# Performance work log

Hardware: AMD Instinct MI355X
Metric: run time of the kernel (lower is better)

Reference implementation:

```python
import jax, jax.numpy as jnp
import numpy as np

B, NB, H, C = 32, 1024, 768, 64


def setup_inputs() -> dict:
    key = jax.random.key(0)
    k1, k2, k3, k4, k5, k6 = jax.random.split(key, 6)
    block_tokens = jax.random.normal(k1, (B, NB, H), dtype=jnp.float32)
    block_active = jax.random.randint(k2, (B, NB), 0, 2) == 1
    block_to_channel_map = jax.random.randint(k3, (NB,), 0, C, dtype=jnp.int64)
    # agg_gate params: Linear(H, H//2) -> Tanh -> Linear(H//2, 1)
    s1 = 1.0 / np.sqrt(H)
    s2 = 1.0 / np.sqrt(H // 2)
    W1 = jax.random.uniform(k4, (H, H // 2), jnp.float32, -s1, s1)
    b1 = jnp.zeros((H // 2,), jnp.float32)
    W2 = jax.random.uniform(k5, (H // 2, 1), jnp.float32, -s2, s2)
    b2 = jnp.zeros((1,), jnp.float32)
    return {"block_tokens": block_tokens, "block_active": block_active,
            "block_to_channel_map": block_to_channel_map,
            "W1": W1, "b1": b1, "W2": W2, "b2": b2}


def reference(block_tokens, block_active, block_to_channel_map, W1, b1, W2, b2):
    # gate MLP: (B, NB)
    h = jnp.tanh(jnp.einsum('bnh,hk->bnk', block_tokens, W1) + b1)
    gate = (jnp.einsum('bnk,ko->bno', h, W2) + b2).squeeze(-1)  # (B, NB)

    # (C, NB) one-hot channel membership; (B, C, NB) active-per-channel mask
    onehot = block_to_channel_map[None, :] == jnp.arange(C)[:, None]
    mask = block_active[:, None, :] & onehot[None, :, :]  # (B, C, NB)

    neg_inf = jnp.float32(-jnp.inf)
    g = jnp.where(mask, gate[:, None, :], neg_inf)  # (B, C, NB)
    m = jnp.max(g, axis=-1, keepdims=True)
    m_safe = jnp.where(jnp.isfinite(m), m, 0.0)  # guard all-masked channels
    e = jnp.where(mask, jnp.exp(g - m_safe), 0.0)
    s = jnp.sum(e, axis=-1, keepdims=True)
    w = jnp.where(s > 0, e / jnp.where(s > 0, s, 1.0), 0.0)  # softmax, nan->0

    channel_tokens = jnp.einsum('bcn,bnh->bch', w, block_tokens)  # (B, C, H)
    channel_active = jnp.any(mask, axis=-1)  # (B, C)
    return channel_tokens, channel_active
```

## Files before the change

### kernel.cpp

```cpp
#include <hip/hip_runtime.h>
#include <math.h>

#define B_    32
#define NB_   1024
#define H_    768
#define K_    384
#define C_    64
#define ROWS_ 32
#define NSTEP_ 24

typedef __attribute__((ext_vector_type(8))) short bf16x8;
typedef __attribute__((ext_vector_type(4))) float f32x4;

__device__ __forceinline__ short f2bf(float f) {
    unsigned u = __float_as_uint(f);
    unsigned r = (u + 0x7fffu + ((u >> 16) & 1u)) >> 16;
    return (short)r;
}
__device__ __forceinline__ float ftanh(float x) {
    float e = __expf(2.f * x);
    return 1.f - 2.f * __builtin_amdgcn_rcpf(e + 1.f);
}

__global__ __launch_bounds__(256) void prep_w1(const float* __restrict__ W1,
                                               short* __restrict__ swz)
{
    int idx = blockIdx.x * 256 + threadIdx.x;
    int k = idx / K_, n = idx % K_;
    float v = W1[idx];
    int s = k >> 5, g = (k >> 3) & 3, i = k & 7;
    int t = n >> 4, nn = n & 15;
    swz[((s * 24 + t) * 512) + (g * 16 + nn) * 8 + i] = f2bf(v);
}

__global__ __launch_bounds__(1024) void compact_kernel(
    const int* __restrict__ active, int* __restrict__ list, int* __restrict__ cnt)
{
    __shared__ int wsum[16];
    __shared__ int wbase[17];
    const int b = blockIdx.x, tid = threadIdx.x, lane = tid & 63, wid = tid >> 6;
    const int flag = active[b * NB_ + tid] != 0;
    const unsigned long long m = __ballot(flag);
    if (lane == 0) wsum[wid] = __popcll(m);
    __syncthreads();
    if (tid == 0) {
        int r = 0;
        for (int i = 0; i < 16; ++i) { wbase[i] = r; r += wsum[i]; }
        wbase[16] = r;
        cnt[b] = r;
    }
    __syncthreads();
    const int total = wbase[16];
    if (flag) {
        const int pos = wbase[wid] + __popcll(m & ((1ull << lane) - 1ull));
        list[b * NB_ + pos] = tid;
    }
    if (tid >= total) list[b * NB_ + tid] = 0;
}

__global__ __launch_bounds__(256, 3) void gate_kernel(
    const float* __restrict__ tokens, const short* __restrict__ swz,
    const float* __restrict__ b1, const float* __restrict__ W2,
    const float* __restrict__ b2, const int* __restrict__ list,
    const int* __restrict__ cnt, float* __restrict__ gate)
{
    __shared__ __align__(16) short As[NSTEP_ * 1024];
    __shared__ float red[4][32];

    const int b = blockIdx.x >> 5;
    const int chunk = blockIdx.x & 31;
    if (chunk * ROWS_ >= cnt[b]) return;

    const int tid = threadIdx.x;
    const int lane = tid & 63;
    const int w = tid >> 6;

    const int r   = tid >> 3;
    const int c8  = tid & 7;
    const int g2w = c8 >> 1, hw = c8 & 1;
    const int fw  = r >> 4,  roww = r & 15;
    const int woff = ((fw * 4 + g2w) * 16 + (roww ^ (g2w << 1))) * 8 + hw * 4;
    const int nrow = list[b * NB_ + chunk * ROWS_ + r];
    const float* aptr = tokens + ((size_t)b * NB_ + nrow) * H_ + c8 * 4;

    const int g2r  = lane >> 4;
    const int rowr = (lane & 15) ^ (g2r << 1);
    const int roff0 = ((0 + g2r) * 16 + rowr) * 8;
    const int roff1 = ((4 + g2r) * 16 + rowr) * 8;

    const short* bbase = swz + (w * 6) * 512 + lane * 8;

    bf16x8 bs[3][6];
#pragma unroll
    for (int j = 0; j < 6; ++j)
        bs[0][j] = *(const bf16x8*)(bbase + 0 * 12288 + j * 512);
#pragma unroll
    for (int j = 0; j < 6; ++j)
        bs[1][j] = *(const bf16x8*)(bbase + 1 * 12288 + j * 512);

#pragma unroll
    for (int g = 0; g < 4; ++g) {
        float4 pa[6];
#pragma unroll
        for (int q = 0; q < 6; ++q)
            pa[q] = *(const float4*)(aptr + (g * 6 + q) * 32);
#pragma unroll
        for (int q = 0; q < 6; ++q) {
            short4 av = {f2bf(pa[q].x), f2bf(pa[q].y), f2bf(pa[q].z), f2bf(pa[q].w)};
            *(short4*)&As[(g * 6 + q) * 1024 + woff] = av;
        }
    }

    f32x4 acc[6][2];
#pragma unroll
    for (int j = 0; j < 6; ++j)
#pragma unroll
        for (int f = 0; f < 2; ++f) acc[j][f] = (f32x4){0.f, 0.f, 0.f, 0.f};

    __syncthreads();

#pragma unroll
    for (int s = 0; s < NSTEP_; ++s) {
        if (s + 2 < NSTEP_) {
            const short* bp = bbase + (size_t)(s + 2) * 12288;
#pragma unroll
            for (int j = 0; j < 6; ++j)
                bs[(s + 2) % 3][j] = *(const bf16x8*)(bp + j * 512);
        }
        bf16x8 a0 = *(const bf16x8*)&As[s * 1024 + roff0];
        bf16x8 a1 = *(const bf16x8*)&As[s * 1024 + roff1];
#pragma unroll
        for (int j = 0; j < 6; ++j) {
            acc[j][0] = __builtin_amdgcn_mfma_f32_16x16x32_bf16(
                            a0, bs[s % 3][j], acc[j][0], 0, 0, 0);
            acc[j][1] = __builtin_amdgcn_mfma_f32_16x16x32_bf16(
                            a1, bs[s % 3][j], acc[j][1], 0, 0, 0);
        }
    }

    float ps[2][4];
#pragma unroll
    for (int f = 0; f < 2; ++f)
#pragma unroll
        for (int rr = 0; rr < 4; ++rr) ps[f][rr] = 0.f;

#pragma unroll
    for (int j = 0; j < 6; ++j) {
        const int n = (w * 6 + j) * 16 + (lane & 15);
        const float bb = b1[n];
        const float ww = W2[n];
#pragma unroll
        for (int f = 0; f < 2; ++f)
#pragma unroll
            for (int rr = 0; rr < 4; ++rr)
                ps[f][rr] += ftanh(acc[j][f][rr] + bb) * ww;
    }
#pragma unroll
    for (int m = 1; m < 16; m <<= 1)
#pragma unroll
        for (int f = 0; f < 2; ++f)
#pragma unroll
            for (int rr = 0; rr < 4; ++rr)
                ps[f][rr] += __shfl_xor(ps[f][rr], m, 64);

    if ((lane & 15) == 0) {
        const int rbase = (lane >> 4) * 4;
#pragma unroll
        for (int f = 0; f < 2; ++f)
#pragma unroll
            for (int rr = 0; rr < 4; ++rr)
                red[w][f * 16 + rbase + rr] = ps[f][rr];
    }
    __syncthreads();
    if (tid < ROWS_) {
        float sg = b2[0];
#pragma unroll
        for (int q = 0; q < 4; ++q) sg += red[q][tid];
        gate[b * NB_ + list[b * NB_ + chunk * ROWS_ + tid]] = sg;
    }
}

__global__ __launch_bounds__(256) void agg_kernel(
    const float* __restrict__ tokens, const int* __restrict__ active,
    const int* __restrict__ cmap, const float* __restrict__ gate,
    float* __restrict__ out_tok, float* __restrict__ out_act)
{
    __shared__ float wls[NB_];
    __shared__ float red[256];
    __shared__ int   idxs[NB_];
    __shared__ float wts[NB_];
    __shared__ int   gbase[17];

    const int b = blockIdx.x >> 6, c = blockIdx.x & 63;
    const int tid = threadIdx.x, lane = tid & 63, wid = tid >> 6;

    float lmax = -INFINITY;
    for (int n = tid; n < NB_; n += 256) {
        const bool msk = (active[b * NB_ + n] != 0) && (cmap[n] == c);
        const float g  = msk ? gate[b * NB_ + n] : -INFINITY;
        wls[n] = g;
        lmax = fmaxf(lmax, g);
    }
    red[tid] = lmax; __syncthreads();
    for (int s = 128; s > 0; s >>= 1) {
        if (tid < s) red[tid] = fmaxf(red[tid], red[tid + s]);
        __syncthreads();
    }
    const float m = red[0]; __syncthreads();
    const float msafe = (m > -INFINITY) ? m : 0.f;

    float lsum = 0.f;
    for (int n = tid; n < NB_; n += 256) {
        const float g = wls[n];
        const float e = (g > -INFINITY) ? __expf(g - msafe) : 0.f;
        wls[n] = e; lsum += e;
    }
    red[tid] = lsum; __syncthreads();
    for (int s = 128; s > 0; s >>= 1) {
        if (tid < s) red[tid] += red[tid + s];
        __syncthreads();
    }
    const float ssum = red[0];
    const float inv  = (ssum > 0.f) ? 1.f / ssum : 0.f;
    __syncthreads();

#pragma unroll
    for (int it = 0; it < 4; ++it) {
        const int n = it * 256 + wid * 64 + lane;
        const unsigned long long mask = __ballot(wls[n] > 0.f);
        if (lane == 0) gbase[1 + it * 4 + wid] = __popcll(mask);
    }
    __syncthreads();
    if (tid == 0) {
        gbase[0] = 0;
        for (int i = 1; i <= 16; ++i) gbase[i] += gbase[i - 1];
    }
    __syncthreads();
#pragma unroll
    for (int it = 0; it < 4; ++it) {
        const int n = it * 256 + wid * 64 + lane;
        const float e = wls[n];
        const unsigned long long mask = __ballot(e > 0.f);
        if (e > 0.f) {
            const int pos = gbase[it * 4 + wid] +
                            __popcll(mask & ((1ull << lane) - 1ull));
            idxs[pos] = n;
            wts[pos]  = e * inv;
        }
    }
    __syncthreads();
    const int cnt = gbase[16];

    if (tid < 192) {
        const int d = tid * 4;
        const float* tb = tokens + (size_t)b * NB_ * H_ + d;
        float4 a = {0.f, 0.f, 0.f, 0.f};
        for (int i = 0; i < cnt; ++i) {
            const float wv = wts[i];
            const float4 v = *(const float4*)(tb + (size_t)idxs[i] * H_);
            a.x += wv * v.x; a.y += wv * v.y;
            a.z += wv * v.z; a.w += wv * v.w;
        }
        *(float4*)(out_tok + ((size_t)(b * C_ + c)) * H_ + d) = a;
    }
    if (tid == 0) out_act[b * C_ + c] = (m > -INFINITY) ? 1.f : 0.f;
}

extern "C" void kernel_launch(void* const* d_in, const int* in_sizes, int n_in,
                              void* d_out, int out_size, void* d_ws, size_t ws_size,
                              hipStream_t stream)
{
    const float* tokens = (const float*)d_in[0];
    const int*   active = (const int*)  d_in[1];
    const int*   cmap   = (const int*)  d_in[2];
    const float* W1     = (const float*)d_in[3];
    const float* b1     = (const float*)d_in[4];
    const float* W2     = (const float*)d_in[5];
    const float* b2     = (const float*)d_in[6];

    float* out      = (float*)d_out;
    float* out_act  = out + (size_t)B_ * C_ * H_;

    short* swz     = (short*)d_ws;
    float* gate_ws = (float*)((char*)d_ws + 589824);
    int*   list    = (int*)  ((char*)d_ws + 720896);
    int*   cntb    = (int*)  ((char*)d_ws + 851968);

    compact_kernel<<<B_, 1024, 0, stream>>>(active, list, cntb);
    prep_w1<<<(H_ * K_) / 256, 256, 0, stream>>>(W1, swz);
    gate_kernel<<<B_ * 32, 256, 0, stream>>>(tokens, swz, b1, W2, b2, list, cntb, gate_ws);
    agg_kernel<<<B_ * C_, 256, 0, stream>>>(tokens, active, cmap, gate_ws, out, out_act);
}
```

Measured before the change: 63.16 us.

## Load gate-MLP A operands directly into registers with a 3-stage prefetch, dropping LDS staging

The gate kernel no longer converts the whole 32x768 token tile into shared memory up front behind a barrier. Each wave now loads its own A fragments from global memory straight into registers, converts them to bf16 just before the MFMA, and prefetches three K-steps ahead alongside the existing B prefetch. The aim is to remove the LDS write/read traffic and the up-front load stall and to overlap the token loads with compute. In exchange, all four waves redundantly read the same token rows from global/L2, and register pressure rises, so occupancy is lowered from 3 to 2 blocks per SM.

```diff
diff --git a/kernel.cpp b/kernel.cpp
--- a/kernel.cpp
+++ b/kernel.cpp
@@ -6,7 +6,6 @@
 #define H_    768
 #define K_    384
 #define C_    64
-#define ROWS_ 32
 #define NSTEP_ 24
 
 typedef __attribute__((ext_vector_type(8))) short bf16x8;
@@ -16,6 +15,11 @@
     unsigned u = __float_as_uint(f);
     unsigned r = (u + 0x7fffu + ((u >> 16) & 1u)) >> 16;
     return (short)r;
+}
+__device__ __forceinline__ bf16x8 cvt8(const float4& a, const float4& b) {
+    bf16x8 v = { f2bf(a.x), f2bf(a.y), f2bf(a.z), f2bf(a.w),
+                 f2bf(b.x), f2bf(b.y), f2bf(b.z), f2bf(b.w) };
+    return v;
 }
 __device__ __forceinline__ float ftanh(float x) {
     float e = __expf(2.f * x);
@@ -58,77 +62,68 @@
     if (tid >= total) list[b * NB_ + tid] = 0;
 }
 
-__global__ __launch_bounds__(256, 3) void gate_kernel(
+__global__ __launch_bounds__(256, 2) void gate_kernel(
     const float* __restrict__ tokens, const short* __restrict__ swz,
     const float* __restrict__ b1, const float* __restrict__ W2,
     const float* __restrict__ b2, const int* __restrict__ list,
     const int* __restrict__ cnt, float* __restrict__ gate)
 {
-    __shared__ __align__(16) short As[NSTEP_ * 1024];
     __shared__ float red[4][32];
 
     const int b = blockIdx.x >> 5;
     const int chunk = blockIdx.x & 31;
-    if (chunk * ROWS_ >= cnt[b]) return;
-
-    const int tid = threadIdx.x;
+    if (chunk * 32 >= cnt[b]) return;
+
+    const int tid  = threadIdx.x;
     const int lane = tid & 63;
-    const int w = tid >> 6;
-
-    const int r   = tid >> 3;
-    const int c8  = tid & 7;
-    const int g2w = c8 >> 1, hw = c8 & 1;
-    const int fw  = r >> 4,  roww = r & 15;
-    const int woff = ((fw * 4 + g2w) * 16 + (roww ^ (g2w << 1))) * 8 + hw * 4;
-    const int nrow = list[b * NB_ + chunk * ROWS_ + r];
-    const float* aptr = tokens + ((size_t)b * NB_ + nrow) * H_ + c8 * 4;
-
-    const int g2r  = lane >> 4;
-    const int rowr = (lane & 15) ^ (g2r << 1);
-    const int roff0 = ((0 + g2r) * 16 + rowr) * 8;
-    const int roff1 = ((4 + g2r) * 16 + rowr) * 8;
-
+    const int w    = tid >> 6;
+    const int lrow = lane & 15;
+    const int kg   = lane >> 4;
+
+    const int n0 = list[b * NB_ + chunk * 32 + lrow];
+    const int n1 = list[b * NB_ + chunk * 32 + 16 + lrow];
+    const float* ap0 = tokens + ((size_t)b * NB_ + n0) * H_ + kg * 8;
+    const float* ap1 = tokens + ((size_t)b * NB_ + n1) * H_ + kg * 8;
     const short* bbase = swz + (w * 6) * 512 + lane * 8;
 
+    f32x4 acc[6][2];
+#pragma unroll
+    for (int j = 0; j < 6; ++j)
+#pragma unroll
+        for (int f = 0; f < 2; ++f) acc[j][f] = (f32x4){0.f, 0.f, 0.f, 0.f};
+
+    float4 pa[3][4];
     bf16x8 bs[3][6];
-#pragma unroll
-    for (int j = 0; j < 6; ++j)
-        bs[0][j] = *(const bf16x8*)(bbase + 0 * 12288 + j * 512);
-#pragma unroll
-    for (int j = 0; j < 6; ++j)
-        bs[1][j] = *(const bf16x8*)(bbase + 1 * 12288 + j * 512);
-
-#pragma unroll
-    for (int g = 0; g < 4; ++g) {
-        float4 pa[6];
-#pragma unroll
-        for (int q = 0; q < 6; ++q)
-            pa[q] = *(const float4*)(aptr + (g * 6 + q) * 32);
-#pragma unroll
-        for (int q = 0; q < 6; ++q) {
-            short4 av = {f2bf(pa[q].x), f2bf(pa[q].y), f2bf(pa[q].z), f2bf(pa[q].w)};
-            *(short4*)&As[(g * 6 + q) * 1024 + woff] = av;
-        }
-    }
-
-    f32x4 acc[6][2];
-#pragma unroll
-    for (int j = 0; j < 6; ++j)
-#pragma unroll
-        for (int f = 0; f < 2; ++f) acc[j][f] = (f32x4){0.f, 0.f, 0.f, 0.f};
-
-    __syncthreads();
+
+#pragma unroll
+    for (int s = 0; s < 3; ++s) {
+        pa[s][0] = *(const float4*)(ap0 + s * 32);
+        pa[s][1] = *(const float4*)(ap0 + s * 32 + 4);
+        pa[s][2] = *(const float4*)(ap1 + s * 32);
+        pa[s][3] = *(const float4*)(ap1 + s * 32 + 4);
+    }
+#pragma unroll
+    for (int s = 0; s < 2; ++s)
+#pragma unroll
+        for (int j = 0; j < 6; ++j)
+            bs[s][j] = *(const bf16x8*)(bbase + s * 12288 + j * 512);
 
 #pragma unroll
     for (int s = 0; s < NSTEP_; ++s) {
+        bf16x8 a0 = cvt8(pa[s % 3][0], pa[s % 3][1]);
+        bf16x8 a1 = cvt8(pa[s % 3][2], pa[s % 3][3]);
+        if (s + 3 < NSTEP_) {
+            pa[s % 3][0] = *(const float4*)(ap0 + (s + 3) * 32);
+            pa[s % 3][1] = *(const float4*)(ap0 + (s + 3) * 32 + 4);
+            pa[s % 3][2] = *(const float4*)(ap1 + (s + 3) * 32);
+            pa[s % 3][3] = *(const float4*)(ap1 + (s + 3) * 32 + 4);
+        }
         if (s + 2 < NSTEP_) {
             const short* bp = bbase + (size_t)(s + 2) * 12288;
 #pragma unroll
             for (int j = 0; j < 6; ++j)
                 bs[(s + 2) % 3][j] = *(const bf16x8*)(bp + j * 512);
         }
-        bf16x8 a0 = *(const bf16x8*)&As[s * 1024 + roff0];
-        bf16x8 a1 = *(const bf16x8*)&As[s * 1024 + roff1];
 #pragma unroll
         for (int j = 0; j < 6; ++j) {
             acc[j][0] = __builtin_amdgcn_mfma_f32_16x16x32_bf16(
@@ -146,7 +141,7 @@
 
 #pragma unroll
     for (int j = 0; j < 6; ++j) {
-        const int n = (w * 6 + j) * 16 + (lane & 15);
+        const int n = (w * 6 + j) * 16 + lrow;
         const float bb = b1[n];
         const float ww = W2[n];
 #pragma unroll
@@ -163,20 +158,19 @@
             for (int rr = 0; rr < 4; ++rr)
                 ps[f][rr] += __shfl_xor(ps[f][rr], m, 64);
 
-    if ((lane & 15) == 0) {
-        const int rbase = (lane >> 4) * 4;
+    if (lrow == 0) {
 #pragma unroll
         for (int f = 0; f < 2; ++f)
 #pragma unroll
             for (int rr = 0; rr < 4; ++rr)
-                red[w][f * 16 + rbase + rr] = ps[f][rr];
-    }
-    __syncthreads();
-    if (tid < ROWS_) {
+                red[w][f * 16 + kg * 4 + rr] = ps[f][rr];
+    }
+    __syncthreads();
+    if (tid < 32) {
         float sg = b2[0];
 #pragma unroll
         for (int q = 0; q < 4; ++q) sg += red[q][tid];
-        gate[b * NB_ + list[b * NB_ + chunk * ROWS_ + tid]] = sg;
+        gate[b * NB_ + list[b * NB_ + chunk * 32 + tid]] = sg;
     }
 }
 
```

After: 90.26 us. 42.9% more time.
